# Kernel optimization log

Hardware: AMD Instinct MI355X
Metric: run time of the kernel (lower is better)

## Reference

```python
import jax, jax.numpy as jnp
import numpy as np

NEG_SLOPE = 0.2


def gatv2(x, src, dst, Wl, Wr, att, b, concat):
    """PyG GATv2Conv (share_weights=False, default negative_slope=0.2).
    x: [N, Fin]; src/dst: [E] (self-loops already included);
    Wl/Wr: [Fin, H*D]; att: [H, D]; b: [H*D] if concat else [D].
    """
    N = x.shape[0]
    H, D = att.shape
    xl = (x @ Wl).reshape(N, H, D)  # source transform (messages)
    xr = (x @ Wr).reshape(N, H, D)  # target transform
    g = xl[src] + xr[dst]                                   # [E, H, D]
    e = jnp.einsum('ehd,hd->eh', jax.nn.leaky_relu(g, NEG_SLOPE), att)  # [E, H]
    # segment softmax over incoming edges of each dst node
    m = jax.ops.segment_max(e, dst, num_segments=N)         # [N, H]
    ex = jnp.exp(e - m[dst])
    s = jax.ops.segment_sum(ex, dst, num_segments=N)
    alpha = ex / (s[dst] + 1e-16)                           # [E, H]
    out = jax.ops.segment_sum(alpha[:, :, None] * xl[src], dst, num_segments=N)  # [N, H, D]
    out = out.reshape(N, H * D) if concat else out.mean(axis=1)
    return out + b


def _glorot(key, fan_in, shape):
    return jax.random.normal(key, shape, dtype=jnp.float32) / np.sqrt(fan_in)


def setup_inputs() -> dict:
    key = jax.random.key(0)
    N, E = 50000, 800000
    dim_in, dim_h, dim_out, heads = 128, 32, 16, 8
    hid = dim_h * heads  # 256
    ks = jax.random.split(key, 16)
    x = jax.random.normal(ks[0], (N, dim_in), dtype=jnp.float32)
    edge_index = jax.random.randint(ks[1], (2, E), 0, N, dtype=jnp.int32)
    p = {
        'Wl1': _glorot(ks[2], dim_in, (dim_in, hid)),
        'Wr1': _glorot(ks[3], dim_in, (dim_in, hid)),
        'att1': _glorot(ks[4], dim_h, (heads, dim_h)),
        'b1': jnp.zeros((hid,), jnp.float32),
        'Wl2': _glorot(ks[5], hid, (hid, hid)),
        'Wr2': _glorot(ks[6], hid, (hid, hid)),
        'att2': _glorot(ks[7], dim_h, (heads, dim_h)),
        'b2': jnp.zeros((hid,), jnp.float32),
        'Wl3': _glorot(ks[8], hid, (hid, hid)),
        'Wr3': _glorot(ks[9], hid, (hid, hid)),
        'att3': _glorot(ks[10], dim_h, (heads, dim_h)),
        'b3': jnp.zeros((hid,), jnp.float32),
        'Wl4': _glorot(ks[11], hid, (hid, dim_out)),
        'Wr4': _glorot(ks[12], hid, (hid, dim_out)),
        'att4': _glorot(ks[13], dim_out, (1, dim_out)),
        'b4': jnp.zeros((dim_out,), jnp.float32),
    }
    return {'x': x, 'edge_index': edge_index, **p}


def reference(x, edge_index,
              Wl1, Wr1, att1, b1,
              Wl2, Wr2, att2, b2,
              Wl3, Wr3, att3, b3,
              Wl4, Wr4, att4, b4):
    N = x.shape[0]
    # PyG GATv2Conv default add_self_loops=True
    loop = jnp.arange(N, dtype=edge_index.dtype)
    src = jnp.concatenate([edge_index[0], loop])
    dst = jnp.concatenate([edge_index[1], loop])
    # eval mode: dropout is identity (note: first dropout output is unused in source)
    h = gatv2(x, src, dst, Wl1, Wr1, att1, b1, concat=True)
    h = jax.nn.elu(h)
    h = gatv2(h, src, dst, Wl2, Wr2, att2, b2, concat=True)
    h = jax.nn.elu(h)
    h = gatv2(h, src, dst, Wl3, Wr3, att3, b3, concat=True)
    h = jax.nn.elu(h)
    h = gatv2(h, src, dst, Wl4, Wr4, att4, b4, concat=True)  # heads=1 -> same as concat
    return jax.nn.log_softmax(h, axis=1)
```

## Files before the change

kernel.cpp:

```cpp
#include <hip/hip_runtime.h>
#include <math.h>

#define NEG_SLOPE 0.2f

typedef _Float16 f16;
typedef _Float16 f16x2 __attribute__((ext_vector_type(2)));
typedef _Float16 f16x4 __attribute__((ext_vector_type(4)));
typedef _Float16 f16x8 __attribute__((ext_vector_type(8)));
typedef float f32x4 __attribute__((ext_vector_type(4)));

static inline int idiv(int a, int b) { return (a + b - 1) / b; }



__global__ __launch_bounds__(256) void conv_x_packed(const float* __restrict__ x,
                                                     f16* __restrict__ pa, int N) {
    int R = blockIdx.x;
    #pragma unroll
    for (int u = 0; u < 8; ++u) {
        int c = threadIdx.x + u * 256;
        int g = c >> 7, r = c & 127;
        int row = R * 128 + r;
        f16x8 v;
        if (row < N) {
            float4 a = *(const float4*)(x + (size_t)row * 128 + g * 8);
            float4 b = *(const float4*)(x + (size_t)row * 128 + g * 8 + 4);
            v = (f16x8){(f16)a.x, (f16)a.y, (f16)a.z, (f16)a.w,
                        (f16)b.x, (f16)b.y, (f16)b.z, (f16)b.w};
        } else {
            v = (f16x8){0, 0, 0, 0, 0, 0, 0, 0};
        }
        *(f16x8*)(pa + ((size_t)(R * 16 + g) * 128 + r) * 8) = v;
    }
}

__global__ __launch_bounds__(256) void convT_all(
    const float* __restrict__ W1l, const float* __restrict__ W1r,
    const float* __restrict__ W2l, const float* __restrict__ W2r,
    const float* __restrict__ W3l, const float* __restrict__ W3r,
    f16* __restrict__ P1l, f16* __restrict__ P1r,
    f16* __restrict__ P2l, f16* __restrict__ P2r,
    f16* __restrict__ P3l, f16* __restrict__ P3r) {
    __shared__ float tbl[32][33];
    const float* W;
    f16* P;
    int K;
    switch (blockIdx.z) {
        case 0: W = W1l; P = P1l; K = 128; break;
        case 1: W = W1r; P = P1r; K = 128; break;
        case 2: W = W2l; P = P2l; K = 256; break;
        case 3: W = W2r; P = P2r; K = 256; break;
        case 4: W = W3l; P = P3l; K = 256; break;
        default: W = W3r; P = P3r; K = 256; break;
    }
    int bk = blockIdx.x * 32, bc = blockIdx.y * 32;
    if (bk >= K) return;
    int tx = threadIdx.x & 31, ty = threadIdx.x >> 5;
    #pragma unroll
    for (int i = 0; i < 32; i += 8)
        tbl[ty + i][tx] = W[(size_t)(bk + ty + i) * 256 + bc + tx];
    __syncthreads();
    if (threadIdx.x < 128) {
        int cl = threadIdx.x & 31;
        int gl = threadIdx.x >> 5;
        int col = bc + cl;
        int g = (bk >> 3) + gl;
        f16x8 v;
        #pragma unroll
        for (int j = 0; j < 8; ++j) v[j] = (f16)tbl[gl * 8 + j][cl];
        *(f16x8*)(P + ((size_t)((col >> 7) * (K >> 3) + g) * 128 + (col & 127)) * 8) = v;
    }
}


__global__ void hist_kernel(const int* __restrict__ dst, int E, int N, int* __restrict__ cnt) {
    int i = blockIdx.x * blockDim.x + threadIdx.x;
    if (i >= E + N) return;
    int d = (i < E) ? dst[i] : (i - E);
    atomicAdd(&cnt[d], 1);
}

__global__ __launch_bounds__(256) void scanA(const int* __restrict__ cnt,
                                             int* __restrict__ bsum, int N) {
    __shared__ int ws[4];
    int tid = threadIdx.x, lane = tid & 63, wid = tid >> 6;
    int i0 = blockIdx.x * 1024 + tid * 4;
    int s = 0;
    if (i0 + 3 < N) {
        int4 v = *(const int4*)(cnt + i0);
        s = v.x + v.y + v.z + v.w;
    } else {
        for (int j = 0; j < 4; ++j)
            if (i0 + j < N) s += cnt[i0 + j];
    }
    #pragma unroll
    for (int o = 1; o < 64; o <<= 1) s += __shfl_xor(s, o);
    if (lane == 0) ws[wid] = s;
    __syncthreads();
    if (tid == 0) bsum[blockIdx.x] = ws[0] + ws[1] + ws[2] + ws[3];
}

__global__ __launch_bounds__(256) void scanB(int* __restrict__ bsum, int nb) {
    __shared__ int ws[4];
    int tid = threadIdx.x, lane = tid & 63, wid = tid >> 6;
    int v = (tid < nb) ? bsum[tid] : 0;
    int incl = v;
    #pragma unroll
    for (int o = 1; o < 64; o <<= 1) {
        int t = __shfl_up(incl, o);
        if (lane >= o) incl += t;
    }
    if (lane == 63) ws[wid] = incl;
    __syncthreads();
    int add = 0;
    for (int w = 0; w < wid; ++w) add += ws[w];
    if (tid < nb) bsum[tid] = add + incl - v;
}

__global__ __launch_bounds__(256) void scanC(const int* __restrict__ cnt,
                                             const int* __restrict__ bsum,
                                             int* __restrict__ rp, int* __restrict__ wofs, int N) {
    __shared__ int ws[4];
    __shared__ int base_s;
    int tid = threadIdx.x, lane = tid & 63, wid = tid >> 6;
    int i0 = blockIdx.x * 1024 + tid * 4;
    int v0 = (i0 + 0 < N) ? cnt[i0 + 0] : 0;
    int v1 = (i0 + 1 < N) ? cnt[i0 + 1] : 0;
    int v2 = (i0 + 2 < N) ? cnt[i0 + 2] : 0;
    int v3 = (i0 + 3 < N) ? cnt[i0 + 3] : 0;
    int t4 = v0 + v1 + v2 + v3;
    int incl = t4;
    #pragma unroll
    for (int o = 1; o < 64; o <<= 1) {
        int t = __shfl_up(incl, o);
        if (lane >= o) incl += t;
    }
    if (lane == 63) ws[wid] = incl;
    if (tid == 0) base_s = bsum[blockIdx.x];
    __syncthreads();
    int wadd = 0;
    for (int w = 0; w < wid; ++w) wadd += ws[w];
    int pre = base_s + wadd + incl - t4;
    int p1 = pre + v0, p2 = p1 + v1, p3 = p2 + v2, p4 = p3 + v3;
    if (i0 + 0 < N) { wofs[i0 + 0] = pre; rp[i0 + 1] = p1; }
    if (i0 + 1 < N) { wofs[i0 + 1] = p1;  rp[i0 + 2] = p2; }
    if (i0 + 2 < N) { wofs[i0 + 2] = p2;  rp[i0 + 3] = p3; }
    if (i0 + 3 < N) { wofs[i0 + 3] = p3;  rp[i0 + 4] = p4; }
    if (blockIdx.x == 0 && tid == 0) rp[0] = 0;
}

__global__ void scatter_kernel(const int* __restrict__ src, const int* __restrict__ dst,
                               int E, int N, int* __restrict__ wofs, int* __restrict__ sorted_src) {
    int i = blockIdx.x * blockDim.x + threadIdx.x;
    if (i >= E + N) return;
    int d, s;
    if (i < E) { d = dst[i]; s = src[i]; } else { d = i - E; s = d; }
    int pos = atomicAdd(&wofs[d], 1);
    sorted_src[pos] = s;
}


__device__ __forceinline__ void gll16(const f16* g, f16* l) {
#if __has_builtin(__builtin_amdgcn_global_load_lds)
    __builtin_amdgcn_global_load_lds((const __attribute__((address_space(1))) void*)g,
                                     (__attribute__((address_space(3))) void*)l, 16, 0, 0);
#else
    *(f16x8*)l = *(const f16x8*)g;
#endif
}

__global__ __launch_bounds__(256) void gemm16_packed(
    const f16* __restrict__ PA, int N, int K,
    const f16* __restrict__ PBl, const f16* __restrict__ PBr,
    f16* __restrict__ Cl, f16* __restrict__ Cr) {
    __shared__ f16 lds[2][2][8192];
    const int nblk = gridDim.x;
    int bid = blockIdx.x;
    int xcd = bid & 7, jj = bid >> 3;
    int nper = nblk >> 3, rem = nblk & 7;
    int slot = (xcd < rem) ? xcd * (nper + 1) + jj
                           : rem * (nper + 1) + (xcd - rem) * nper + jj;
    int R = slot >> 2, by = slot & 3;
    const f16* __restrict__ PB = (by >> 1) ? PBr : PBl;
    f16* __restrict__ C = (by >> 1) ? Cr : Cl;
    const int cb = by & 1;
    const int row0 = R * 128;
    const int col0 = cb * 128;
    const f16* Abase = PA + (size_t)R * 128 * K;
    const f16* Bbase = PB + (size_t)cb * 128 * K;
    const int t = threadIdx.x;
    const int lane = t & 63, wid = t >> 6;
    const int wr = (wid >> 1) * 64, wc = (wid & 1) * 64;
    const int lg = lane >> 4, lr = lane & 15;

    f32x4 acc[4][4];
    #pragma unroll
    for (int m = 0; m < 4; ++m)
        #pragma unroll
        for (int n = 0; n < 4; ++n) acc[m][n] = (f32x4){0.f, 0.f, 0.f, 0.f};

    auto stage = [&](int buf, int k0) {
        const f16* As = Abase + (size_t)k0 * 128 + t * 8;
        const f16* Bs = Bbase + (size_t)k0 * 128 + t * 8;
        f16* Al = &lds[buf][0][t * 8];
        f16* Bl = &lds[buf][1][t * 8];
        #pragma unroll
        for (int u = 0; u < 4; ++u) gll16(As + u * 2048, Al + u * 2048);
        #pragma unroll
        for (int u = 0; u < 4; ++u) gll16(Bs + u * 2048, Bl + u * 2048);
    };

    const int nk = K >> 6;
    stage(0, 0);
    asm volatile("s_waitcnt vmcnt(0)" ::: "memory");
    __syncthreads();
    for (int c = 0; c < nk; ++c) {
        if (c + 1 < nk) stage((c + 1) & 1, (c + 1) * 64);
        f16x8* Asp = (f16x8*)lds[c & 1][0];
        f16x8* Bsp = (f16x8*)lds[c & 1][1];
        #pragma unroll
        for (int s = 0; s < 2; ++s) {
            f16x8 af[4], bf[4];
            #pragma unroll
            for (int m = 0; m < 4; ++m) af[m] = Asp[(s * 4 + lg) * 128 + wr + m * 16 + lr];
            #pragma unroll
            for (int n = 0; n < 4; ++n) bf[n] = Bsp[(s * 4 + lg) * 128 + wc + n * 16 + lr];
            #pragma unroll
            for (int m = 0; m < 4; ++m)
                #pragma unroll
                for (int n = 0; n < 4; ++n)
                    acc[m][n] = __builtin_amdgcn_mfma_f32_16x16x32_f16(af[m], bf[n], acc[m][n], 0, 0, 0);
        }
        asm volatile("s_waitcnt vmcnt(0)" ::: "memory");
        __syncthreads();
    }
    const size_t hs = (size_t)N * 32;
    #pragma unroll
    for (int m = 0; m < 4; ++m) {
        int row_b = row0 + wr + m * 16 + lg * 4;
        #pragma unroll
        for (int reg = 0; reg < 4; ++reg) {
            int row = row_b + reg;
            if (row < N) {
                #pragma unroll
                for (int n = 0; n < 4; ++n) {
                    int col = col0 + wc + n * 16 + lr;
                    C[hs * (col >> 5) + (size_t)row * 32 + (col & 31)] = (f16)acc[m][n][reg];
                }
            }
        }
    }
}


__global__ __launch_bounds__(256) void gemm_small16(
    const f16* __restrict__ A, int N,
    const float* __restrict__ Wl, const float* __restrict__ Wr,
    float* __restrict__ Cl, float* __restrict__ Cr) {
    const int K = 256, M = 16;
    __shared__ float As[16][260];
    __shared__ float Ws[256 * 16];
    const float* __restrict__ W = (blockIdx.y == 0) ? Wl : Wr;
    float* __restrict__ C = (blockIdx.y == 0) ? Cl : Cr;
    int row0 = blockIdx.x * 16;
    int tid = threadIdx.x;
    {
        #pragma unroll
        for (int u = 0; u < 4; ++u)
            *(float4*)&Ws[tid * 16 + u * 4] = *(const float4*)(W + tid * 16 + u * 4);
        int r = tid >> 4;
        int c = (tid & 15) * 16;
        int row = row0 + r;
        if (row < N) {
            int R = row >> 7, rr = row & 127;
            const f16* base = A + ((size_t)(R * 32 + (c >> 3)) * 128 + rr) * 8;
            f16x8 v0 = *(const f16x8*)base;
            f16x8 v1 = *(const f16x8*)(base + 1024);
            #pragma unroll
            for (int j = 0; j < 8; ++j) {
                As[r][c + j] = (float)v0[j];
                As[r][c + 8 + j] = (float)v1[j];
            }
        } else {
            #pragma unroll
            for (int j = 0; j < 16; ++j) As[r][c + j] = 0.f;
        }
    }
    __syncthreads();
    int r = tid >> 4;
    int col = tid & 15;
    float acc = 0.f;
    #pragma unroll 8
    for (int k = 0; k < K; ++k) acc = fmaf(As[r][k], Ws[k * M + col], acc);
    int row = row0 + r;
    if (row < N) C[(size_t)row * M + col] = acc;
}


__global__ __launch_bounds__(256) void edge_h8_ns(
    const f16* __restrict__ xl, const f16* __restrict__ xr,
    const int* __restrict__ rp, const int* __restrict__ ss,
    const float* __restrict__ att, const float* __restrict__ bias,
    f16* __restrict__ hout, int N) {
    int bid = blockIdx.x;
    int h = bid & 7;
    int tile = bid >> 3;
    int tid = threadIdx.x;
    int n = tile * 64 + (tid >> 2);
    if (n >= N) return;
    int ll = tid & 3;
    const size_t hs = (size_t)N * 32;
    const f16* xlh = xl + hs * h;
    const int doff = h * 32 + ll * 8;
    f16x8 xrr = *(const f16x8*)(xr + hs * h + (size_t)n * 32 + ll * 8);
    float4 atlo = *(const float4*)(att + doff);
    float4 athi = *(const float4*)(att + doff + 4);
    f16x2 at01 = {(f16)atlo.x, (f16)atlo.y};
    f16x2 at23 = {(f16)atlo.z, (f16)atlo.w};
    f16x2 at45 = {(f16)athi.x, (f16)athi.y};
    f16x2 at67 = {(f16)athi.z, (f16)athi.w};
    const f16 ns = (f16)NEG_SLOPE;
    float m = -INFINITY, s = 0.f;
    f16x8 a = {0, 0, 0, 0, 0, 0, 0, 0};
    int beg = rp[n], end = rp[n + 1];
    int last = end - 1;
    const f16* xb = xlh + ll * 8;
    f16x8 r0 = *(const f16x8*)(xb + (size_t)ss[beg] * 32);
    f16x8 r1 = *(const f16x8*)(xb + (size_t)ss[min(beg + 1, last)] * 32);
    f16x8 r2 = *(const f16x8*)(xb + (size_t)ss[min(beg + 2, last)] * 32);
    f16x8 r3 = *(const f16x8*)(xb + (size_t)ss[min(beg + 3, last)] * 32);
    int j4 = ss[min(beg + 4, last)];
    int j5 = ss[min(beg + 5, last)];

    auto score = [&](const f16x8& cur) -> float {
        f16x8 g = cur + xrr;
        f16x8 gs = g * ns;
        f16x8 lk = __builtin_elementwise_max(g, gs);
#if __has_builtin(__builtin_amdgcn_fdot2)
        f16x2 l01 = __builtin_shufflevector(lk, lk, 0, 1);
        f16x2 l23 = __builtin_shufflevector(lk, lk, 2, 3);
        f16x2 l45 = __builtin_shufflevector(lk, lk, 4, 5);
        f16x2 l67 = __builtin_shufflevector(lk, lk, 6, 7);
        float p = __builtin_amdgcn_fdot2(l01, at01, 0.f, false);
        p = __builtin_amdgcn_fdot2(l23, at23, p, false);
        p = __builtin_amdgcn_fdot2(l45, at45, p, false);
        p = __builtin_amdgcn_fdot2(l67, at67, p, false);
#else
        float p = (float)lk[0] * atlo.x + (float)lk[1] * atlo.y +
                  (float)lk[2] * atlo.z + (float)lk[3] * atlo.w +
                  (float)lk[4] * athi.x + (float)lk[5] * athi.y +
                  (float)lk[6] * athi.z + (float)lk[7] * athi.w;
#endif
        return p;
    };

    int i = beg;
    for (; i + 1 < end; i += 2) {
        f16x8 c0 = r0, c1 = r1;
        r0 = r2; r1 = r3;
        r2 = *(const f16x8*)(xb + (size_t)j4 * 32);
        r3 = *(const f16x8*)(xb + (size_t)j5 * 32);
        j4 = ss[min(i + 6, last)];
        j5 = ss[min(i + 7, last)];
        float p0 = score(c0);
        float p1 = score(c1);
        p0 += __shfl_xor(p0, 1);
        p1 += __shfl_xor(p1, 1);
        p0 += __shfl_xor(p0, 2);
        p1 += __shfl_xor(p1, 2);
        float d0 = p0 - m, d1 = p1 - m;
        if (__any(fmaxf(d0, d1) > 4.f)) {
            float mn = fmaxf(m, fmaxf(p0, p1));
            float cf = __expf(m - mn);
            s *= cf;
            f16 cfh = (f16)cf;
            a = a * (f16x8){cfh, cfh, cfh, cfh, cfh, cfh, cfh, cfh};
            m = mn;
            d0 = p0 - m; d1 = p1 - m;
        }
        float e0 = __expf(d0);
        float e1 = __expf(d1);
        s += e0 + e1;
        f16 e0h = (f16)e0, e1h = (f16)e1;
        f16x8 e0v = {e0h, e0h, e0h, e0h, e0h, e0h, e0h, e0h};
        f16x8 e1v = {e1h, e1h, e1h, e1h, e1h, e1h, e1h, e1h};
#if __has_builtin(__builtin_elementwise_fma)
        a = __builtin_elementwise_fma(c0, e0v, a);
        a = __builtin_elementwise_fma(c1, e1v, a);
#else
        a = a + c0 * e0v + c1 * e1v;
#endif
    }
    if (i < end) {
        f16x8 c0 = r0;
        float p0 = score(c0);
        p0 += __shfl_xor(p0, 1);
        p0 += __shfl_xor(p0, 2);
        float d0 = p0 - m;
        if (__any(d0 > 4.f)) {
            float mn = fmaxf(m, p0);
            float cf = __expf(m - mn);
            s *= cf;
            f16 cfh = (f16)cf;
            a = a * (f16x8){cfh, cfh, cfh, cfh, cfh, cfh, cfh, cfh};
            m = mn;
            d0 = p0 - m;
        }
        float e0 = __expf(d0);
        s += e0;
        f16 e0h = (f16)e0;
        f16x8 e0v = {e0h, e0h, e0h, e0h, e0h, e0h, e0h, e0h};
#if __has_builtin(__builtin_elementwise_fma)
        a = __builtin_elementwise_fma(c0, e0v, a);
#else
        a = a + c0 * e0v;
#endif
    }
    float inv = 1.f / (s + 1e-16f);
    float4 blo = *(const float4*)(bias + doff);
    float4 bhi = *(const float4*)(bias + doff + 4);
    float o[8];
    o[0] = (float)a[0] * inv + blo.x; o[1] = (float)a[1] * inv + blo.y;
    o[2] = (float)a[2] * inv + blo.z; o[3] = (float)a[3] * inv + blo.w;
    o[4] = (float)a[4] * inv + bhi.x; o[5] = (float)a[5] * inv + bhi.y;
    o[6] = (float)a[6] * inv + bhi.z; o[7] = (float)a[7] * inv + bhi.w;
    f16x8 ov;
    #pragma unroll
    for (int j = 0; j < 8; ++j) {
        float e = o[j] > 0.f ? o[j] : __expf(o[j]) - 1.f;
        ov[j] = (f16)e;
    }
    *(f16x8*)(hout + ((size_t)((n >> 7) * 32 + 4 * h + ll) * 128 + (n & 127)) * 8) = ov;
}


__global__ __launch_bounds__(256) void edge_h1_kernel(
    const float* __restrict__ xl, const float* __restrict__ xr,
    const int* __restrict__ rp, const int* __restrict__ ss,
    const float* __restrict__ att, const float* __restrict__ bias,
    float* __restrict__ out, int N) {
    int tid = threadIdx.x;
    int grp = tid >> 4;
    int gl = tid & 15;
    int n = blockIdx.x * 16 + grp;
    if (n >= N) return;
    float xrv = xr[(size_t)n * 16 + gl];
    float attv = att[gl];
    float bv = bias[gl];
    float m = -INFINITY, s = 0.f, acc = 0.f;
    int beg = rp[n], end = rp[n + 1], last = end - 1;
    const float* xb = xl + gl;
    float x0 = xb[(size_t)ss[beg] * 16];
    float x1 = xb[(size_t)ss[min(beg + 1, last)] * 16];
    float x2 = xb[(size_t)ss[min(beg + 2, last)] * 16];
    float x3 = xb[(size_t)ss[min(beg + 3, last)] * 16];
    int j4 = ss[min(beg + 4, last)];
    int j5 = ss[min(beg + 5, last)];
    int i = beg;
    for (; i + 1 < end; i += 2) {
        float c0 = x0, c1 = x1;
        x0 = x2; x1 = x3;
        x2 = xb[(size_t)j4 * 16];
        x3 = xb[(size_t)j5 * 16];
        j4 = ss[min(i + 6, last)];
        j5 = ss[min(i + 7, last)];
        float g0 = c0 + xrv, g1 = c1 + xrv;
        float p0 = attv * fmaxf(g0, NEG_SLOPE * g0);
        float p1 = attv * fmaxf(g1, NEG_SLOPE * g1);
        p0 += __shfl_xor(p0, 1); p1 += __shfl_xor(p1, 1);
        p0 += __shfl_xor(p0, 2); p1 += __shfl_xor(p1, 2);
        p0 += __shfl_xor(p0, 4); p1 += __shfl_xor(p1, 4);
        p0 += __shfl_xor(p0, 8); p1 += __shfl_xor(p1, 8);
        float d0 = p0 - m, d1 = p1 - m;
        if (__any(fmaxf(d0, d1) > 8.f)) {
            float mn = fmaxf(m, fmaxf(p0, p1));
            float cf = __expf(m - mn);
            s *= cf; acc *= cf;
            m = mn;
            d0 = p0 - m; d1 = p1 - m;
        }
        float e0 = __expf(d0), e1 = __expf(d1);
        s += e0 + e1;
        acc = fmaf(e1, c1, fmaf(e0, c0, acc));
    }
    if (i < end) {
        float c0 = x0;
        float g0 = c0 + xrv;
        float p0 = attv * fmaxf(g0, NEG_SLOPE * g0);
        p0 += __shfl_xor(p0, 1);
        p0 += __shfl_xor(p0, 2);
        p0 += __shfl_xor(p0, 4);
        p0 += __shfl_xor(p0, 8);
        float d0 = p0 - m;
        if (__any(d0 > 8.f)) {
            float mn = fmaxf(m, p0);
            float cf = __expf(m - mn);
            s *= cf; acc *= cf;
            m = mn;
            d0 = p0 - m;
        }
        float e0 = __expf(d0);
        s += e0;
        acc = fmaf(e0, c0, acc);
    }
    float v = acc / (s + 1e-16f) + bv;
    float mx = v;
    mx = fmaxf(mx, __shfl_xor(mx, 1));
    mx = fmaxf(mx, __shfl_xor(mx, 2));
    mx = fmaxf(mx, __shfl_xor(mx, 4));
    mx = fmaxf(mx, __shfl_xor(mx, 8));
    float ex = __expf(v - mx);
    float se = ex;
    se += __shfl_xor(se, 1);
    se += __shfl_xor(se, 2);
    se += __shfl_xor(se, 4);
    se += __shfl_xor(se, 8);
    out[(size_t)n * 16 + gl] = v - mx - __logf(se);
}


extern "C" void kernel_launch(void* const* d_in, const int* in_sizes, int n_in,
                              void* d_out, int out_size, void* d_ws, size_t ws_size,
                              hipStream_t stream) {
    const float* x    = (const float*)d_in[0];
    const int*   ei   = (const int*)d_in[1];
    const float* Wl1  = (const float*)d_in[2];
    const float* Wr1  = (const float*)d_in[3];
    const float* att1 = (const float*)d_in[4];
    const float* b1   = (const float*)d_in[5];
    const float* Wl2  = (const float*)d_in[6];
    const float* Wr2  = (const float*)d_in[7];
    const float* att2 = (const float*)d_in[8];
    const float* b2   = (const float*)d_in[9];
    const float* Wl3  = (const float*)d_in[10];
    const float* Wr3  = (const float*)d_in[11];
    const float* att3 = (const float*)d_in[12];
    const float* b3   = (const float*)d_in[13];
    const float* Wl4  = (const float*)d_in[14];
    const float* Wr4  = (const float*)d_in[15];
    const float* att4 = (const float*)d_in[16];
    const float* b4   = (const float*)d_in[17];

    const int N = in_sizes[0] / 128;
    const int E = in_sizes[1] / 2;
    const int* src = ei;
    const int* dst = ei + E;
    const int Etot = E + N;
    const int ntile = idiv(N, 128);

    char* wsb = (char*)d_ws;
    size_t off = 0;
    auto alloc = [&](size_t bytes) -> void* {
        void* p = wsb + off;
        off += (bytes + 255) & ~(size_t)255;
        return p;
    };
    f16*   PX   = (f16*)alloc((size_t)ntile * 128 * 128 * 2);
    f16*   PH   = (f16*)alloc((size_t)ntile * 128 * 256 * 2);
    f16*   xl16 = (f16*)alloc((size_t)N * 256 * 2);
    f16*   xr16 = (f16*)alloc((size_t)N * 256 * 2);
    float* xl4  = (float*)alloc((size_t)N * 16 * 4);
    float* xr4  = (float*)alloc((size_t)N * 16 * 4);
    f16*   PB1l = (f16*)alloc((size_t)256 * 128 * 2);
    f16*   PB1r = (f16*)alloc((size_t)256 * 128 * 2);
    f16*   PB2l = (f16*)alloc((size_t)256 * 256 * 2);
    f16*   PB2r = (f16*)alloc((size_t)256 * 256 * 2);
    f16*   PB3l = (f16*)alloc((size_t)256 * 256 * 2);
    f16*   PB3r = (f16*)alloc((size_t)256 * 256 * 2);
    int*   cnt  = (int*)alloc((size_t)N * 4);
    int*   wof  = (int*)alloc((size_t)N * 4);
    int*   rp   = (int*)alloc((size_t)(N + 1) * 4);
    int*   ss   = (int*)alloc((size_t)Etot * 4);
    int*   bsum = (int*)alloc((size_t)idiv(N, 1024) * 4);

    conv_x_packed<<<ntile, 256, 0, stream>>>(x, PX, N);
    convT_all<<<dim3(8, 8, 6), 256, 0, stream>>>(Wl1, Wr1, Wl2, Wr2, Wl3, Wr3,
                                                 PB1l, PB1r, PB2l, PB2r, PB3l, PB3r);

    hipMemsetAsync(cnt, 0, (size_t)N * 4, stream);
    hist_kernel<<<idiv(Etot, 256), 256, 0, stream>>>(dst, E, N, cnt);
    const int nb = idiv(N, 1024);
    scanA<<<nb, 256, 0, stream>>>(cnt, bsum, N);
    scanB<<<1, 256, 0, stream>>>(bsum, nb);
    scanC<<<nb, 256, 0, stream>>>(cnt, bsum, rp, wof, N);
    scatter_kernel<<<idiv(Etot, 256), 256, 0, stream>>>(src, dst, E, N, wof, ss);

    const int nblk = ntile * 4;
    const int egrid = idiv(N, 64) * 8;
    gemm16_packed<<<nblk, 256, 0, stream>>>(PX, N, 128, PB1l, PB1r, xl16, xr16);
    edge_h8_ns<<<egrid, 256, 0, stream>>>(xl16, xr16, rp, ss, att1, b1, PH, N);
    gemm16_packed<<<nblk, 256, 0, stream>>>(PH, N, 256, PB2l, PB2r, xl16, xr16);
    edge_h8_ns<<<egrid, 256, 0, stream>>>(xl16, xr16, rp, ss, att2, b2, PH, N);
    gemm16_packed<<<nblk, 256, 0, stream>>>(PH, N, 256, PB3l, PB3r, xl16, xr16);
    edge_h8_ns<<<egrid, 256, 0, stream>>>(xl16, xr16, rp, ss, att3, b3, PH, N);
    gemm_small16<<<dim3(idiv(N, 16), 2), 256, 0, stream>>>(PH, N, Wl4, Wr4, xl4, xr4);
    edge_h1_kernel<<<idiv(N, 16), 256, 0, stream>>>(xl4, xr4, rp, ss, att4, b4,
                                                    (float*)d_out, N);
}
```

Measured before the change: 437.4 us.

## Load GEMM fragments directly from global and batch multiple nodes per edge thread

The fp16 MFMA GEMM stops staging A/B tiles through LDS with global_load_lds and double buffering. Each lane now loads its MFMA fragments straight from the packed global layout into registers, with a two-step register prefetch, which removes the LDS traffic and the block barriers. The edge aggregation kernels (8-head and 1-head) now have each thread group loop over 4 nodes, with grids shrunk by 4x, to amortise setup such as att/bias loads and launch overhead. The costs are more redundant global/L2 fragment reads across waves that previously shared LDS tiles, and fewer blocks available to hide gather latency.

```diff
diff --git a/kernel.cpp b/kernel.cpp
--- a/kernel.cpp
+++ b/kernel.cpp
@@ -160,20 +160,10 @@
 }
 
 
-__device__ __forceinline__ void gll16(const f16* g, f16* l) {
-#if __has_builtin(__builtin_amdgcn_global_load_lds)
-    __builtin_amdgcn_global_load_lds((const __attribute__((address_space(1))) void*)g,
-                                     (__attribute__((address_space(3))) void*)l, 16, 0, 0);
-#else
-    *(f16x8*)l = *(const f16x8*)g;
-#endif
-}
-
-__global__ __launch_bounds__(256) void gemm16_packed(
+__global__ __launch_bounds__(256) void gemm16_direct(
     const f16* __restrict__ PA, int N, int K,
     const f16* __restrict__ PBl, const f16* __restrict__ PBr,
     f16* __restrict__ Cl, f16* __restrict__ Cr) {
-    __shared__ f16 lds[2][2][8192];
     const int nblk = gridDim.x;
     int bid = blockIdx.x;
     int xcd = bid & 7, jj = bid >> 3;
@@ -186,53 +176,52 @@
     const int cb = by & 1;
     const int row0 = R * 128;
     const int col0 = cb * 128;
-    const f16* Abase = PA + (size_t)R * 128 * K;
-    const f16* Bbase = PB + (size_t)cb * 128 * K;
     const int t = threadIdx.x;
     const int lane = t & 63, wid = t >> 6;
     const int wr = (wid >> 1) * 64, wc = (wid & 1) * 64;
     const int lg = lane >> 4, lr = lane & 15;
 
+    const f16* Ap = PA + (size_t)R * 128 * K + ((size_t)lg * 128 + wr + lr) * 8;
+    const f16* Bp = PB + (size_t)cb * 128 * K + ((size_t)lg * 128 + wc + lr) * 8;
+
     f32x4 acc[4][4];
     #pragma unroll
     for (int m = 0; m < 4; ++m)
         #pragma unroll
         for (int n = 0; n < 4; ++n) acc[m][n] = (f32x4){0.f, 0.f, 0.f, 0.f};
 
-    auto stage = [&](int buf, int k0) {
-        const f16* As = Abase + (size_t)k0 * 128 + t * 8;
-        const f16* Bs = Bbase + (size_t)k0 * 128 + t * 8;
-        f16* Al = &lds[buf][0][t * 8];
-        f16* Bl = &lds[buf][1][t * 8];
-        #pragma unroll
-        for (int u = 0; u < 4; ++u) gll16(As + u * 2048, Al + u * 2048);
-        #pragma unroll
-        for (int u = 0; u < 4; ++u) gll16(Bs + u * 2048, Bl + u * 2048);
-    };
-
-    const int nk = K >> 6;
-    stage(0, 0);
-    asm volatile("s_waitcnt vmcnt(0)" ::: "memory");
-    __syncthreads();
-    for (int c = 0; c < nk; ++c) {
-        if (c + 1 < nk) stage((c + 1) & 1, (c + 1) * 64);
-        f16x8* Asp = (f16x8*)lds[c & 1][0];
-        f16x8* Bsp = (f16x8*)lds[c & 1][1];
-        #pragma unroll
-        for (int s = 0; s < 2; ++s) {
-            f16x8 af[4], bf[4];
+    f16x8 afA[4], bfA[4], afB[4], bfB[4];
+    #pragma unroll
+    for (int mm = 0; mm < 4; ++mm) {
+        afA[mm] = *(const f16x8*)(Ap + mm * 128);
+        bfA[mm] = *(const f16x8*)(Bp + mm * 128);
+    }
+    const int ncs = K >> 5;
+    for (int cs = 0; cs < ncs; cs += 2) {
+        size_t o1 = (size_t)(cs + 1) * 4096;
+        #pragma unroll
+        for (int mm = 0; mm < 4; ++mm) {
+            afB[mm] = *(const f16x8*)(Ap + o1 + mm * 128);
+            bfB[mm] = *(const f16x8*)(Bp + o1 + mm * 128);
+        }
+        #pragma unroll
+        for (int m = 0; m < 4; ++m)
             #pragma unroll
-            for (int m = 0; m < 4; ++m) af[m] = Asp[(s * 4 + lg) * 128 + wr + m * 16 + lr];
+            for (int n = 0; n < 4; ++n)
+                acc[m][n] = __builtin_amdgcn_mfma_f32_16x16x32_f16(afA[m], bfA[n], acc[m][n], 0, 0, 0);
+        if (cs + 2 < ncs) {
+            size_t o2 = (size_t)(cs + 2) * 4096;
             #pragma unroll
-            for (int n = 0; n < 4; ++n) bf[n] = Bsp[(s * 4 + lg) * 128 + wc + n * 16 + lr];
+            for (int mm = 0; mm < 4; ++mm) {
+                afA[mm] = *(const f16x8*)(Ap + o2 + mm * 128);
+                bfA[mm] = *(const f16x8*)(Bp + o2 + mm * 128);
+            }
+        }
+        #pragma unroll
+        for (int m = 0; m < 4; ++m)
             #pragma unroll
-            for (int m = 0; m < 4; ++m)
-                #pragma unroll
-                for (int n = 0; n < 4; ++n)
-                    acc[m][n] = __builtin_amdgcn_mfma_f32_16x16x32_f16(af[m], bf[n], acc[m][n], 0, 0, 0);
-        }
-        asm volatile("s_waitcnt vmcnt(0)" ::: "memory");
-        __syncthreads();
+            for (int n = 0; n < 4; ++n)
+                acc[m][n] = __builtin_amdgcn_mfma_f32_16x16x32_f16(afB[m], bfB[n], acc[m][n], 0, 0, 0);
     }
     const size_t hs = (size_t)N * 32;
     #pragma unroll
@@ -297,7 +286,7 @@
 }
 
 
-__global__ __launch_bounds__(256) void edge_h8_ns(
+__global__ __launch_bounds__(256) void edge_h8_b4(
     const f16* __restrict__ xl, const f16* __restrict__ xr,
     const int* __restrict__ rp, const int* __restrict__ ss,
     const float* __restrict__ att, const float* __restrict__ bias,
@@ -306,33 +295,25 @@
     int h = bid & 7;
     int tile = bid >> 3;
     int tid = threadIdx.x;
-    int n = tile * 64 + (tid >> 2);
-    if (n >= N) return;
+    int wv = tid >> 6;
+    int gw = (tid >> 2) & 15;
     int ll = tid & 3;
+    int wbase = tile * 256 + wv * 64;
     const size_t hs = (size_t)N * 32;
     const f16* xlh = xl + hs * h;
     const int doff = h * 32 + ll * 8;
-    f16x8 xrr = *(const f16x8*)(xr + hs * h + (size_t)n * 32 + ll * 8);
+    const f16* xb = xlh + ll * 8;
     float4 atlo = *(const float4*)(att + doff);
     float4 athi = *(const float4*)(att + doff + 4);
     f16x2 at01 = {(f16)atlo.x, (f16)atlo.y};
     f16x2 at23 = {(f16)atlo.z, (f16)atlo.w};
     f16x2 at45 = {(f16)athi.x, (f16)athi.y};
     f16x2 at67 = {(f16)athi.z, (f16)athi.w};
+    float4 blo = *(const float4*)(bias + doff);
+    float4 bhi = *(const float4*)(bias + doff + 4);
     const f16 ns = (f16)NEG_SLOPE;
-    float m = -INFINITY, s = 0.f;
-    f16x8 a = {0, 0, 0, 0, 0, 0, 0, 0};
-    int beg = rp[n], end = rp[n + 1];
-    int last = end - 1;
-    const f16* xb = xlh + ll * 8;
-    f16x8 r0 = *(const f16x8*)(xb + (size_t)ss[beg] * 32);
-    f16x8 r1 = *(const f16x8*)(xb + (size_t)ss[min(beg + 1, last)] * 32);
-    f16x8 r2 = *(const f16x8*)(xb + (size_t)ss[min(beg + 2, last)] * 32);
-    f16x8 r3 = *(const f16x8*)(xb + (size_t)ss[min(beg + 3, last)] * 32);
-    int j4 = ss[min(beg + 4, last)];
-    int j5 = ss[min(beg + 5, last)];
-
-    auto score = [&](const f16x8& cur) -> float {
+
+    auto score = [&](const f16x8& cur, const f16x8& xrr) -> float {
         f16x8 g = cur + xrr;
         f16x8 gs = g * ns;
         f16x8 lk = __builtin_elementwise_max(g, gs);
@@ -354,83 +335,98 @@
         return p;
     };
 
-    int i = beg;
-    for (; i + 1 < end; i += 2) {
-        f16x8 c0 = r0, c1 = r1;
-        r0 = r2; r1 = r3;
-        r2 = *(const f16x8*)(xb + (size_t)j4 * 32);
-        r3 = *(const f16x8*)(xb + (size_t)j5 * 32);
-        j4 = ss[min(i + 6, last)];
-        j5 = ss[min(i + 7, last)];
-        float p0 = score(c0);
-        float p1 = score(c1);
-        p0 += __shfl_xor(p0, 1);
-        p1 += __shfl_xor(p1, 1);
-        p0 += __shfl_xor(p0, 2);
-        p1 += __shfl_xor(p1, 2);
-        float d0 = p0 - m, d1 = p1 - m;
-        if (__any(fmaxf(d0, d1) > 4.f)) {
-            float mn = fmaxf(m, fmaxf(p0, p1));
-            float cf = __expf(m - mn);
-            s *= cf;
-            f16 cfh = (f16)cf;
-            a = a * (f16x8){cfh, cfh, cfh, cfh, cfh, cfh, cfh, cfh};
-            m = mn;
-            d0 = p0 - m; d1 = p1 - m;
-        }
-        float e0 = __expf(d0);
-        float e1 = __expf(d1);
-        s += e0 + e1;
-        f16 e0h = (f16)e0, e1h = (f16)e1;
-        f16x8 e0v = {e0h, e0h, e0h, e0h, e0h, e0h, e0h, e0h};
-        f16x8 e1v = {e1h, e1h, e1h, e1h, e1h, e1h, e1h, e1h};
+    #pragma unroll 1
+    for (int tt = 0; tt < 4; ++tt) {
+        int n = wbase + tt * 16 + gw;
+        if (n >= N) continue;
+        f16x8 xrr = *(const f16x8*)(xr + hs * h + (size_t)n * 32 + ll * 8);
+        float m = -INFINITY, s = 0.f;
+        f16x8 a = {0, 0, 0, 0, 0, 0, 0, 0};
+        int beg = rp[n], end = rp[n + 1];
+        int last = end - 1;
+        f16x8 r0 = *(const f16x8*)(xb + (size_t)ss[beg] * 32);
+        f16x8 r1 = *(const f16x8*)(xb + (size_t)ss[min(beg + 1, last)] * 32);
+        f16x8 r2 = *(const f16x8*)(xb + (size_t)ss[min(beg + 2, last)] * 32);
+        f16x8 r3 = *(const f16x8*)(xb + (size_t)ss[min(beg + 3, last)] * 32);
+        int j4 = ss[min(beg + 4, last)];
+        int j5 = ss[min(beg + 5, last)];
+
+        int i = beg;
+        for (; i + 1 < end; i += 2) {
+            f16x8 c0 = r0, c1 = r1;
+            r0 = r2; r1 = r3;
+            r2 = *(const f16x8*)(xb + (size_t)j4 * 32);
+            r3 = *(const f16x8*)(xb + (size_t)j5 * 32);
+            j4 = ss[min(i + 6, last)];
+            j5 = ss[min(i + 7, last)];
+            float p0 = score(c0, xrr);
+            float p1 = score(c1, xrr);
+            p0 += __shfl_xor(p0, 1);
+            p1 += __shfl_xor(p1, 1);
+            p0 += __shfl_xor(p0, 2);
+            p1 += __shfl_xor(p1, 2);
+            float d0 = p0 - m, d1 = p1 - m;
+            if (__any(fmaxf(d0, d1) > 4.f)) {
+                float mn = fmaxf(m, fmaxf(p0, p1));
+                float cf = __expf(m - mn);
+                s *= cf;
+                f16 cfh = (f16)cf;
+                a = a * (f16x8){cfh, cfh, cfh, cfh, cfh, cfh, cfh, cfh};
+                m = mn;
+                d0 = p0 - m; d1 = p1 - m;
+            }
+            float e0 = __expf(d0);
+            float e1 = __expf(d1);
+            s += e0 + e1;
+            f16 e0h = (f16)e0, e1h = (f16)e1;
+            f16x8 e0v = {e0h, e0h, e0h, e0h, e0h, e0h, e0h, e0h};
+            f16x8 e1v = {e1h, e1h, e1h, e1h, e1h, e1h, e1h, e1h};
 #if __has_builtin(__builtin_elementwise_fma)
-        a = __builtin_elementwise_fma(c0, e0v, a);
-        a = __builtin_elementwise_fma(c1, e1v, a);
+            a = __builtin_elementwise_fma(c0, e0v, a);
+            a = __builtin_elementwise_fma(c1, e1v, a);
 #else
-        a = a + c0 * e0v + c1 * e1v;
+            a = a + c0 * e0v + c1 * e1v;
 #endif
-    }
-    if (i < end) {
-        f16x8 c0 = r0;
-        float p0 = score(c0);
-        p0 += __shfl_xor(p0, 1);
-        p0 += __shfl_xor(p0, 2);
-        float d0 = p0 - m;
-        if (__any(d0 > 4.f)) {
-            float mn = fmaxf(m, p0);
-            float cf = __expf(m - mn);
-            s *= cf;
-            f16 cfh = (f16)cf;
-            a = a * (f16x8){cfh, cfh, cfh, cfh, cfh, cfh, cfh, cfh};
-            m = mn;
-            d0 = p0 - m;
-        }
-        float e0 = __expf(d0);
-        s += e0;
-        f16 e0h = (f16)e0;
-        f16x8 e0v = {e0h, e0h, e0h, e0h, e0h, e0h, e0h, e0h};
+        }
+        if (i < end) {
+            f16x8 c0 = r0;
+            float p0 = score(c0, xrr);
+            p0 += __shfl_xor(p0, 1);
+            p0 += __shfl_xor(p0, 2);
+            float d0 = p0 - m;
+            if (__any(d0 > 4.f)) {
+                float mn = fmaxf(m, p0);
+                float cf = __expf(m - mn);
+                s *= cf;
+                f16 cfh = (f16)cf;
+                a = a * (f16x8){cfh, cfh, cfh, cfh, cfh, cfh, cfh, cfh};
+                m = mn;
+                d0 = p0 - m;
+            }
+            float e0 = __expf(d0);
+            s += e0;
+            f16 e0h = (f16)e0;
+            f16x8 e0v = {e0h, e0h, e0h, e0h, e0h, e0h, e0h, e0h};
 #if __has_builtin(__builtin_elementwise_fma)
-        a = __builtin_elementwise_fma(c0, e0v, a);
+            a = __builtin_elementwise_fma(c0, e0v, a);
 #else
-        a = a + c0 * e0v;
+            a = a + c0 * e0v;
 #endif
-    }
-    float inv = 1.f / (s + 1e-16f);
-    float4 blo = *(const float4*)(bias + doff);
-    float4 bhi = *(const float4*)(bias + doff + 4);
-    float o[8];
-    o[0] = (float)a[0] * inv + blo.x; o[1] = (float)a[1] * inv + blo.y;
-    o[2] = (float)a[2] * inv + blo.z; o[3] = (float)a[3] * inv + blo.w;
-    o[4] = (float)a[4] * inv + bhi.x; o[5] = (float)a[5] * inv + bhi.y;
-    o[6] = (float)a[6] * inv + bhi.z; o[7] = (float)a[7] * inv + bhi.w;
-    f16x8 ov;
-    #pragma unroll
-    for (int j = 0; j < 8; ++j) {
-        float e = o[j] > 0.f ? o[j] : __expf(o[j]) - 1.f;
-        ov[j] = (f16)e;
-    }
-    *(f16x8*)(hout + ((size_t)((n >> 7) * 32 + 4 * h + ll) * 128 + (n & 127)) * 8) = ov;
+        }
+        float inv = 1.f / (s + 1e-16f);
+        float o[8];
+        o[0] = (float)a[0] * inv + blo.x; o[1] = (float)a[1] * inv + blo.y;
+        o[2] = (float)a[2] * inv + blo.z; o[3] = (float)a[3] * inv + blo.w;
+        o[4] = (float)a[4] * inv + bhi.x; o[5] = (float)a[5] * inv + bhi.y;
+        o[6] = (float)a[6] * inv + bhi.z; o[7] = (float)a[7] * inv + bhi.w;
+        f16x8 ov;
+        #pragma unroll
+        for (int j = 0; j < 8; ++j) {
+            float e = o[j] > 0.f ? o[j] : __expf(o[j]) - 1.f;
+            ov[j] = (f16)e;
+        }
+        *(f16x8*)(hout + ((size_t)((n >> 7) * 32 + 4 * h + ll) * 128 + (n & 127)) * 8) = ov;
+    }
 }
 
 
@@ -440,82 +436,87 @@
     const float* __restrict__ att, const float* __restrict__ bias,
     float* __restrict__ out, int N) {
     int tid = threadIdx.x;
-    int grp = tid >> 4;
+    int wv = tid >> 6;
+    int gw = (tid >> 4) & 3;
     int gl = tid & 15;
-    int n = blockIdx.x * 16 + grp;
-    if (n >= N) return;
-    float xrv = xr[(size_t)n * 16 + gl];
+    int wbase = blockIdx.x * 64 + wv * 16;
     float attv = att[gl];
     float bv = bias[gl];
-    float m = -INFINITY, s = 0.f, acc = 0.f;
-    int beg = rp[n], end = rp[n + 1], last = end - 1;
     const float* xb = xl + gl;
-    float x0 = xb[(size_t)ss[beg] * 16];
-    float x1 = xb[(size_t)ss[min(beg + 1, last)] * 16];
-    float x2 = xb[(size_t)ss[min(beg + 2, last)] * 16];
-    float x3 = xb[(size_t)ss[min(beg + 3, last)] * 16];
-    int j4 = ss[min(beg + 4, last)];
-    int j5 = ss[min(beg + 5, last)];
-    int i = beg;
-    for (; i + 1 < end; i += 2) {
-        float c0 = x0, c1 = x1;
-        x0 = x2; x1 = x3;
-        x2 = xb[(size_t)j4 * 16];
-        x3 = xb[(size_t)j5 * 16];
-        j4 = ss[min(i + 6, last)];
-        j5 = ss[min(i + 7, last)];
-        float g0 = c0 + xrv, g1 = c1 + xrv;
-        float p0 = attv * fmaxf(g0, NEG_SLOPE * g0);
-        float p1 = attv * fmaxf(g1, NEG_SLOPE * g1);
-        p0 += __shfl_xor(p0, 1); p1 += __shfl_xor(p1, 1);
-        p0 += __shfl_xor(p0, 2); p1 += __shfl_xor(p1, 2);
-        p0 += __shfl_xor(p0, 4); p1 += __shfl_xor(p1, 4);
-        p0 += __shfl_xor(p0, 8); p1 += __shfl_xor(p1, 8);
-        float d0 = p0 - m, d1 = p1 - m;
-        if (__any(fmaxf(d0, d1) > 8.f)) {
-            float mn = fmaxf(m, fmaxf(p0, p1));
-            float cf = __expf(m - mn);
-            s *= cf; acc *= cf;
-            m = mn;
-            d0 = p0 - m; d1 = p1 - m;
-        }
-        float e0 = __expf(d0), e1 = __expf(d1);
-        s += e0 + e1;
-        acc = fmaf(e1, c1, fmaf(e0, c0, acc));
-    }
-    if (i < end) {
-        float c0 = x0;
-        float g0 = c0 + xrv;
-        float p0 = attv * fmaxf(g0, NEG_SLOPE * g0);
-        p0 += __shfl_xor(p0, 1);
-        p0 += __shfl_xor(p0, 2);
-        p0 += __shfl_xor(p0, 4);
-        p0 += __shfl_xor(p0, 8);
-        float d0 = p0 - m;
-        if (__any(d0 > 8.f)) {
-            float mn = fmaxf(m, p0);
-            float cf = __expf(m - mn);
-            s *= cf; acc *= cf;
-            m = mn;
-            d0 = p0 - m;
-        }
-        float e0 = __expf(d0);
-        s += e0;
-        acc = fmaf(e0, c0, acc);
-    }
-    float v = acc / (s + 1e-16f) + bv;
-    float mx = v;
-    mx = fmaxf(mx, __shfl_xor(mx, 1));
-    mx = fmaxf(mx, __shfl_xor(mx, 2));
-    mx = fmaxf(mx, __shfl_xor(mx, 4));
-    mx = fmaxf(mx, __shfl_xor(mx, 8));
-    float ex = __expf(v - mx);
-    float se = ex;
-    se += __shfl_xor(se, 1);
-    se += __shfl_xor(se, 2);
-    se += __shfl_xor(se, 4);
-    se += __shfl_xor(se, 8);
-    out[(size_t)n * 16 + gl] = v - mx - __logf(se);
+    #pragma unroll 1
+    for (int tt = 0; tt < 4; ++tt) {
+        int n = wbase + tt * 4 + gw;
+        if (n >= N) continue;
+        float xrv = xr[(size_t)n * 16 + gl];
+        float m = -INFINITY, s = 0.f, acc = 0.f;
+        int beg = rp[n], end = rp[n + 1], last = end - 1;
+        float x0 = xb[(size_t)ss[beg] * 16];
+        float x1 = xb[(size_t)ss[min(beg + 1, last)] * 16];
+        float x2 = xb[(size_t)ss[min(beg + 2, last)] * 16];
+        float x3 = xb[(size_t)ss[min(beg + 3, last)] * 16];
+        int j4 = ss[min(beg + 4, last)];
+        int j5 = ss[min(beg + 5, last)];
+        int i = beg;
+        for (; i + 1 < end; i += 2) {
+            float c0 = x0, c1 = x1;
+            x0 = x2; x1 = x3;
+            x2 = xb[(size_t)j4 * 16];
+            x3 = xb[(size_t)j5 * 16];
+            j4 = ss[min(i + 6, last)];
+            j5 = ss[min(i + 7, last)];
+            float g0 = c0 + xrv, g1 = c1 + xrv;
+            float p0 = attv * fmaxf(g0, NEG_SLOPE * g0);
+            float p1 = attv * fmaxf(g1, NEG_SLOPE * g1);
+            p0 += __shfl_xor(p0, 1); p1 += __shfl_xor(p1, 1);
+            p0 += __shfl_xor(p0, 2); p1 += __shfl_xor(p1, 2);
+            p0 += __shfl_xor(p0, 4); p1 += __shfl_xor(p1, 4);
+            p0 += __shfl_xor(p0, 8); p1 += __shfl_xor(p1, 8);
+            float d0 = p0 - m, d1 = p1 - m;
+            if (__any(fmaxf(d0, d1) > 8.f)) {
+                float mn = fmaxf(m, fmaxf(p0, p1));
+                float cf = __expf(m - mn);
+                s *= cf; acc *= cf;
+                m = mn;
+                d0 = p0 - m; d1 = p1 - m;
+            }
+            float e0 = __expf(d0), e1 = __expf(d1);
+            s += e0 + e1;
+            acc = fmaf(e1, c1, fmaf(e0, c0, acc));
+        }
+        if (i < end) {
+            float c0 = x0;
+            float g0 = c0 + xrv;
+            float p0 = attv * fmaxf(g0, NEG_SLOPE * g0);
+            p0 += __shfl_xor(p0, 1);
+            p0 += __shfl_xor(p0, 2);
+            p0 += __shfl_xor(p0, 4);
+            p0 += __shfl_xor(p0, 8);
+            float d0 = p0 - m;
+            if (__any(d0 > 8.f)) {
+                float mn = fmaxf(m, p0);
+                float cf = __expf(m - mn);
+                s *= cf; acc *= cf;
+                m = mn;
+                d0 = p0 - m;
+            }
+            float e0 = __expf(d0);
+            s += e0;
+            acc = fmaf(e0, c0, acc);
+        }
+        float v = acc / (s + 1e-16f) + bv;
+        float mx = v;
+        mx = fmaxf(mx, __shfl_xor(mx, 1));
+        mx = fmaxf(mx, __shfl_xor(mx, 2));
+        mx = fmaxf(mx, __shfl_xor(mx, 4));
+        mx = fmaxf(mx, __shfl_xor(mx, 8));
+        float ex = __expf(v - mx);
+        float se = ex;
+        se += __shfl_xor(se, 1);
+        se += __shfl_xor(se, 2);
+        se += __shfl_xor(se, 4);
+        se += __shfl_xor(se, 8);
+        out[(size_t)n * 16 + gl] = v - mx - __logf(se);
+    }
 }
 
 
@@ -586,14 +587,14 @@
     scatter_kernel<<<idiv(Etot, 256), 256, 0, stream>>>(src, dst, E, N, wof, ss);
 
     const int nblk = ntile * 4;
-    const int egrid = idiv(N, 64) * 8;
-    gemm16_packed<<<nblk, 256, 0, stream>>>(PX, N, 128, PB1l, PB1r, xl16, xr16);
-    edge_h8_ns<<<egrid, 256, 0, stream>>>(xl16, xr16, rp, ss, att1, b1, PH, N);
-    gemm16_packed<<<nblk, 256, 0, stream>>>(PH, N, 256, PB2l, PB2r, xl16, xr16);
-    edge_h8_ns<<<egrid, 256, 0, stream>>>(xl16, xr16, rp, ss, att2, b2, PH, N);
-    gemm16_packed<<<nblk, 256, 0, stream>>>(PH, N, 256, PB3l, PB3r, xl16, xr16);
-    edge_h8_ns<<<egrid, 256, 0, stream>>>(xl16, xr16, rp, ss, att3, b3, PH, N);
+    const int egrid = idiv(N, 256) * 8;
+    gemm16_direct<<<nblk, 256, 0, stream>>>(PX, N, 128, PB1l, PB1r, xl16, xr16);
+    edge_h8_b4<<<egrid, 256, 0, stream>>>(xl16, xr16, rp, ss, att1, b1, PH, N);
+    gemm16_direct<<<nblk, 256, 0, stream>>>(PH, N, 256, PB2l, PB2r, xl16, xr16);
+    edge_h8_b4<<<egrid, 256, 0, stream>>>(xl16, xr16, rp, ss, att2, b2, PH, N);
+    gemm16_direct<<<nblk, 256, 0, stream>>>(PH, N, 256, PB3l, PB3r, xl16, xr16);
+    edge_h8_b4<<<egrid, 256, 0, stream>>>(xl16, xr16, rp, ss, att3, b3, PH, N);
     gemm_small16<<<dim3(idiv(N, 16), 2), 256, 0, stream>>>(PH, N, Wl4, Wr4, xl4, xr4);
-    edge_h1_kernel<<<idiv(N, 16), 256, 0, stream>>>(xl4, xr4, rp, ss, att4, b4,
+    edge_h1_kernel<<<idiv(N, 64), 256, 0, stream>>>(xl4, xr4, rp, ss, att4, b4,
                                                     (float*)d_out, N);
 }
```

Result: slower. 473.9 us (+8.3%).
